# Performance work log

Hardware: AMD Instinct MI355X
Metric: run time of the kernel (lower is better)

The kernel has to match this reference:

```python
import jax, jax.numpy as jnp
import numpy as np

N_NODES = 100000
N_EDGES = 3200000
IN_CH = 128
HID_CH = 64
NEG_SLOPE = 0.2  # PyG GATConv default leaky_relu slope


def setup_inputs() -> dict:
    key = jax.random.key(0)
    k1, k2, k3, k4, k5, k6 = jax.random.split(key, 6)
    x = jax.random.normal(k1, (N_NODES, IN_CH), dtype=jnp.float32)
    edge_index = jax.random.randint(k2, (2, N_EDGES), 0, N_NODES, dtype=jnp.int64)
    # learned params of GATConv(in, hid, heads=1)
    W = jax.random.normal(k3, (IN_CH, HID_CH), dtype=jnp.float32) / np.sqrt(IN_CH)
    att_src = jax.random.normal(k4, (HID_CH,), dtype=jnp.float32) / np.sqrt(HID_CH)
    att_dst = jax.random.normal(k5, (HID_CH,), dtype=jnp.float32) / np.sqrt(HID_CH)
    bias = jax.random.normal(k6, (HID_CH,), dtype=jnp.float32) * 0.01
    return {"x": x, "edge_index": edge_index, "W": W, "att_src": att_src,
            "att_dst": att_dst, "bias": bias}


def reference(x, edge_index, W, att_src, att_dst, bias):
    N = x.shape[0]
    h = x @ W  # [N, H] linear transform
    # PyG GATConv default: add self loops
    loops = jnp.arange(N, dtype=edge_index.dtype)
    src = jnp.concatenate([edge_index[0], loops])  # [E+N]
    dst = jnp.concatenate([edge_index[1], loops])
    # per-node attention halves, then gather per-edge
    a_src = h @ att_src  # [N]
    a_dst = h @ att_dst  # [N]
    e = jax.nn.leaky_relu(a_src[src] + a_dst[dst], NEG_SLOPE)  # [E+N]
    # segment softmax over incoming edges of each destination node
    m = jax.ops.segment_max(e, dst, num_segments=N)
    e = jnp.exp(e - m[dst])
    s = jax.ops.segment_sum(e, dst, num_segments=N)
    alpha = e / s[dst]  # [E+N]
    # scatter-aggregate weighted source features
    out = jax.ops.segment_sum(h[src] * alpha[:, None], dst, num_segments=N) + bias
    return out, alpha[:, None]
```

## Files before the change

kernel.cpp:

```cpp
#include <hip/hip_runtime.h>
#include <hip/hip_bf16.h>

#define IN_CH 128
#define HID 64
#define NEG_SLOPE 0.2f
#define BSH 8
#define CAP 10240

typedef __attribute__((ext_vector_type(8))) short short8;
typedef __attribute__((ext_vector_type(4))) float floatx4;
typedef __attribute__((ext_vector_type(2))) float f32x2;

__device__ inline short bfr(float f) {
    unsigned u = __float_as_uint(f);
    u += 0x7fffu + ((u >> 16) & 1u);
    return (short)(u >> 16);
}

__global__ void k_prep(const float* __restrict__ W, short* __restrict__ wfrag,
                       int* __restrict__ g_cursor)
{
    if (blockIdx.x == 0) {
        g_cursor[threadIdx.x] = 0;
        g_cursor[threadIdx.x + 256] = 0;
    }
    int idx = blockIdx.x * 256 + threadIdx.x;
    if (idx >= 1024) return;
    int f = idx >> 6, l = idx & 63;
    int kt = f >> 2, nt = f & 3;
    int k0 = kt * 32 + (l >> 4) * 8;
    int n = nt * 16 + (l & 15);
#pragma unroll
    for (int j = 0; j < 8; ++j)
        wfrag[idx * 8 + j] = bfr(W[(k0 + j) * HID + n]);
}

__global__ __launch_bounds__(256) void k_gemm(
    const float* __restrict__ x, const short8* __restrict__ wfrag,
    const float* __restrict__ att_src, const float* __restrict__ att_dst,
    short* __restrict__ h, float* __restrict__ a_src,
    float* __restrict__ a_dst, int N)
{
    const int t = threadIdx.x;
    const int lane = t & 63;
    const int wv = t >> 6;
    const int l15 = lane & 15;
    const int quad = lane >> 4;

    short8 bf[16];
#pragma unroll
    for (int f = 0; f < 16; ++f) bf[f] = wfrag[f * 64 + lane];

    float as4[4], ad4[4];
#pragma unroll
    for (int nt = 0; nt < 4; ++nt) {
        as4[nt] = att_src[nt * 16 + l15];
        ad4[nt] = att_dst[nt * 16 + l15];
    }

    const int rowbase = blockIdx.x * 128 + wv * 32;

#pragma unroll
    for (int mt = 0; mt < 2; ++mt) {
        const int m0 = rowbase + mt * 16;
        const int rowa = m0 + l15;
        const int rowc = rowa < N ? rowa : N - 1;
        const float* xp = x + (size_t)rowc * IN_CH + quad * 8;

        short8 af[4];
#pragma unroll
        for (int kt = 0; kt < 4; ++kt) {
            float4 p0 = *(const float4*)(xp + kt * 32);
            float4 p1 = *(const float4*)(xp + kt * 32 + 4);
            short8 a;
            a[0] = bfr(p0.x); a[1] = bfr(p0.y); a[2] = bfr(p0.z); a[3] = bfr(p0.w);
            a[4] = bfr(p1.x); a[5] = bfr(p1.y); a[6] = bfr(p1.z); a[7] = bfr(p1.w);
            af[kt] = a;
        }

        floatx4 acc[4];
#pragma unroll
        for (int nt = 0; nt < 4; ++nt) acc[nt] = (floatx4){0.f, 0.f, 0.f, 0.f};
#pragma unroll
        for (int kt = 0; kt < 4; ++kt)
#pragma unroll
            for (int nt = 0; nt < 4; ++nt)
                acc[nt] = __builtin_amdgcn_mfma_f32_16x16x32_bf16(
                    af[kt], bf[kt * 4 + nt], acc[nt], 0, 0, 0);

#pragma unroll
        for (int r = 0; r < 4; ++r) {
            const int row = m0 + quad * 4 + r;
            const bool ok = row < N;
            if (ok) {
#pragma unroll
                for (int nt = 0; nt < 4; ++nt)
                    h[(size_t)row * HID + nt * 16 + l15] = bfr(acc[nt][r]);
            }
            float ps = acc[0][r] * as4[0] + acc[1][r] * as4[1] +
                       acc[2][r] * as4[2] + acc[3][r] * as4[3];
            float pd = acc[0][r] * ad4[0] + acc[1][r] * ad4[1] +
                       acc[2][r] * ad4[2] + acc[3][r] * ad4[3];
#pragma unroll
            for (int m2 = 1; m2 < 16; m2 <<= 1) {
                ps += __shfl_xor(ps, m2, 64);
                pd += __shfl_xor(pd, m2, 64);
            }
            if (ok && l15 == 0) { a_src[row] = ps; a_dst[row] = pd; }
        }
    }
}

__global__ __launch_bounds__(512) void k_binB(
    const int* __restrict__ ei, int* __restrict__ g_cursor,
    int* __restrict__ pairs, int E, int nb)
{
    __shared__ int hist[512];
    __shared__ int base[512];
    const int t = threadIdx.x;
    hist[t] = 0;
    __syncthreads();

    int s[8], d[8], l[8];
    const int4* s4 = (const int4*)ei;
    const int4* d4 = (const int4*)(ei + E);
    const int E4 = E >> 2;
    const int q0 = blockIdx.x * 1024;
#pragma unroll
    for (int i = 0; i < 2; ++i) {
        int q = q0 + i * 512 + t;
        int4 sv = make_int4(0, 0, 0, 0);
        int4 dv = make_int4(-1, -1, -1, -1);
        if (q < E4) { sv = s4[q]; dv = d4[q]; }
        s[4 * i + 0] = sv.x; s[4 * i + 1] = sv.y; s[4 * i + 2] = sv.z; s[4 * i + 3] = sv.w;
        d[4 * i + 0] = dv.x; d[4 * i + 1] = dv.y; d[4 * i + 2] = dv.z; d[4 * i + 3] = dv.w;
    }
#pragma unroll
    for (int i = 0; i < 8; ++i)
        if (d[i] >= 0) l[i] = atomicAdd(&hist[d[i] >> BSH], 1);
    __syncthreads();

    if (t < nb) base[t] = atomicAdd(&g_cursor[t], hist[t]);
    __syncthreads();

#pragma unroll
    for (int i = 0; i < 8; ++i) {
        if (d[i] < 0) continue;
        int b = d[i] >> BSH;
        int pos = base[b] + l[i];
        if (pos < CAP)
            pairs[b * CAP + pos] = s[i] | ((d[i] & 255) << 17);
    }
}

__global__ __launch_bounds__(512) void k_binC(
    const int* __restrict__ pairs, const int* __restrict__ g_cursor,
    int* __restrict__ row_start, int* __restrict__ cnt,
    int* __restrict__ csr_src, int N, int nb)
{
    __shared__ int h0[256];
    __shared__ int hs[512];
    __shared__ int cur[256];
    __shared__ int sbase;
    const int t = threadIdx.x;
    const int b = blockIdx.x;
    int m = g_cursor[b];
    if (m > CAP) m = CAP;
    const int4* pb4 = (const int4*)(pairs + b * CAP);
    const int m4 = (m + 3) >> 2;

    int bv = (t < nb) ? g_cursor[t] : 0;
    hs[t] = bv;
    __syncthreads();
    for (int off = 1; off < 512; off <<= 1) {
        int u = (t >= off) ? hs[t - off] : 0;
        __syncthreads();
        hs[t] += u;
        __syncthreads();
    }
    if (t == b) sbase = hs[t] - bv;
    if (t < 256) h0[t] = 0;
    __syncthreads();
    const int basec = sbase;

    for (int i4 = t; i4 < m4; i4 += 512) {
        const int4 p = pb4[i4];
        const int i = i4 << 2;
        if (i + 3 < m) {
            atomicAdd(&h0[p.x >> 17], 1);
            atomicAdd(&h0[p.y >> 17], 1);
            atomicAdd(&h0[p.z >> 17], 1);
            atomicAdd(&h0[p.w >> 17], 1);
        } else {
            if (i     < m) atomicAdd(&h0[p.x >> 17], 1);
            if (i + 1 < m) atomicAdd(&h0[p.y >> 17], 1);
            if (i + 2 < m) atomicAdd(&h0[p.z >> 17], 1);
        }
    }
    __syncthreads();

    if (t < 256) hs[t] = h0[t];
    __syncthreads();
    for (int off = 1; off < 256; off <<= 1) {
        int u = (t >= off && t < 256) ? hs[t - off] : 0;
        __syncthreads();
        if (t < 256) hs[t] += u;
        __syncthreads();
    }
    if (t < 256) {
        const int excl = hs[t] - h0[t];
        cur[t] = basec + excl;
        const int dd = (b << BSH) + t;
        if (dd < N) { row_start[dd] = basec + excl; cnt[dd] = h0[t]; }
    }
    __syncthreads();

    for (int i4 = t; i4 < m4; i4 += 512) {
        const int4 p = pb4[i4];
        const int i = i4 << 2;
        if (i < m) {
            int pos = atomicAdd(&cur[p.x >> 17], 1);
            csr_src[pos] = p.x & 0x1FFFF;
        }
        if (i + 1 < m) {
            int pos = atomicAdd(&cur[p.y >> 17], 1);
            csr_src[pos] = p.y & 0x1FFFF;
        }
        if (i + 2 < m) {
            int pos = atomicAdd(&cur[p.z >> 17], 1);
            csr_src[pos] = p.z & 0x1FFFF;
        }
        if (i + 3 < m) {
            int pos = atomicAdd(&cur[p.w >> 17], 1);
            csr_src[pos] = p.w & 0x1FFFF;
        }
    }
}

__global__ __launch_bounds__(256) void k_agg(
    const __hip_bfloat16* __restrict__ h, const float* __restrict__ a_src,
    const float* __restrict__ a_dst, const float* __restrict__ bias,
    const int* __restrict__ row_start, const int* __restrict__ cnt,
    const int* __restrict__ csr_src,
    float* __restrict__ out, float2* __restrict__ adi, int dbase, int N)
{
    __shared__ float red[4][2][576];

    const int wave = threadIdx.x >> 6;
    const int lane = threadIdx.x & 63;
    const int d0 = dbase + blockIdx.x * 8 + wave * 2;
    if (d0 >= N) return;
    const int d1 = d0 + 1;
    const bool has1 = d1 < N;

    const int q  = lane >> 3;
    const int i8 = lane & 7;

    const float2 ad2 = *(const float2*)(a_dst + d0);
    const float ad0 = ad2.x;
    const float ad1 = ad2.y;
    const int2 cn2 = *(const int2*)(cnt + d0);
    const int n0 = cn2.x;
    const int n1 = has1 ? cn2.y : 0;
    const int st0 = row_start[d0];
    const int en0 = st0 + n0;
    const int st1 = en0;
    const int en1 = st1 + n1;

    const uint4* h4 = (const uint4*)h;

    float ps0 = 0.f, ps1 = 0.f;
    f32x2 ac0[4], ac1[4];
#pragma unroll
    for (int c = 0; c < 4; ++c) {
        ac0[c] = (f32x2){0.f, 0.f};
        ac1[c] = (f32x2){0.f, 0.f};
    }

    const int nbt0 = (n0 + 63) >> 6;
    const int nbt1 = (n1 + 63) >> 6;
    const int nbm = nbt0 > nbt1 ? nbt0 : nbt1;

    int b0 = st0, b1 = st1;
    for (int it = 0; it < nbm; ++it, b0 += 64, b1 += 64) {
        int s0v = 0, s1v = 0;
        float e0 = 0.f, e1 = 0.f;
        const int idx0 = b0 + lane;
        if (it < nbt0 && idx0 < en0) {
            s0v = csr_src[idx0];
            float v = a_src[s0v] + ad0;
            v = v > 0.f ? v : NEG_SLOPE * v;
            e0 = __expf(v);
            ps0 += e0;
        }
        const int idx1 = b1 + lane;
        if (it < nbt1 && idx1 < en1) {
            s1v = csr_src[idx1];
            float v = a_src[s1v] + ad1;
            v = v > 0.f ? v : NEG_SLOPE * v;
            e1 = __expf(v);
            ps1 += e1;
        }
        const int m0 = (it < nbt0) ? min(64, en0 - b0) : 0;
        const int m1 = (it < nbt1) ? min(64, en1 - b1) : 0;
        const int mm = m0 > m1 ? m0 : m1;
#pragma unroll 4
        for (int j = 0; j < mm; j += 8) {
            const int jq = j + q;
            const int sj0 = __shfl(s0v, jq, 64);
            const float ej0 = __shfl(e0, jq, 64);
            const int sj1 = __shfl(s1v, jq, 64);
            const float ej1 = __shfl(e1, jq, 64);
            uint4 u0 = h4[(size_t)sj0 * 8 + i8];
            uint4 u1 = h4[(size_t)sj1 * 8 + i8];
            f32x2 ev0; ev0[0] = ej0; ev0[1] = ej0;
            f32x2 ev1; ev1[0] = ej1; ev1[1] = ej1;
            f32x2 c;
            c[0] = __uint_as_float(u0.x << 16);
            c[1] = __uint_as_float(u0.x & 0xffff0000u);
            ac0[0] = __builtin_elementwise_fma(ev0, c, ac0[0]);
            c[0] = __uint_as_float(u0.y << 16);
            c[1] = __uint_as_float(u0.y & 0xffff0000u);
            ac0[1] = __builtin_elementwise_fma(ev0, c, ac0[1]);
            c[0] = __uint_as_float(u0.z << 16);
            c[1] = __uint_as_float(u0.z & 0xffff0000u);
            ac0[2] = __builtin_elementwise_fma(ev0, c, ac0[2]);
            c[0] = __uint_as_float(u0.w << 16);
            c[1] = __uint_as_float(u0.w & 0xffff0000u);
            ac0[3] = __builtin_elementwise_fma(ev0, c, ac0[3]);
            c[0] = __uint_as_float(u1.x << 16);
            c[1] = __uint_as_float(u1.x & 0xffff0000u);
            ac1[0] = __builtin_elementwise_fma(ev1, c, ac1[0]);
            c[0] = __uint_as_float(u1.y << 16);
            c[1] = __uint_as_float(u1.y & 0xffff0000u);
            ac1[1] = __builtin_elementwise_fma(ev1, c, ac1[1]);
            c[0] = __uint_as_float(u1.z << 16);
            c[1] = __uint_as_float(u1.z & 0xffff0000u);
            ac1[2] = __builtin_elementwise_fma(ev1, c, ac1[2]);
            c[0] = __uint_as_float(u1.w << 16);
            c[1] = __uint_as_float(u1.w & 0xffff0000u);
            ac1[3] = __builtin_elementwise_fma(ev1, c, ac1[3]);
        }
    }

    float* r0 = &red[wave][0][0];
    float* r1 = &red[wave][1][0];
#pragma unroll
    for (int p = 0; p < 4; ++p) {
        r0[(i8 * 8 + 2 * p) * 9 + q]     = ac0[p][0];
        r0[(i8 * 8 + 2 * p + 1) * 9 + q] = ac0[p][1];
        r1[(i8 * 8 + 2 * p) * 9 + q]     = ac1[p][0];
        r1[(i8 * 8 + 2 * p + 1) * 9 + q] = ac1[p][1];
    }

#pragma unroll
    for (int m2 = 32; m2 > 0; m2 >>= 1) {
        ps0 += __shfl_xor(ps0, m2, 64);
        ps1 += __shfl_xor(ps1, m2, 64);
    }

    const float2 asd = *(const float2*)(a_src + d0);
    float vs0 = asd.x + ad0;
    vs0 = vs0 > 0.f ? vs0 : NEG_SLOPE * vs0;
    const float es0 = __expf(vs0);
    const float inv0 = 1.f / (ps0 + es0);
    float es1 = 0.f, inv1 = 0.f;
    if (has1) {
        float vs1 = asd.y + ad1;
        vs1 = vs1 > 0.f ? vs1 : NEG_SLOPE * vs1;
        es1 = __expf(vs1);
        inv1 = 1.f / (ps1 + es1);
    }
    if (lane == 0) {
        adi[d0] = make_float2(ad0, inv0);
        if (has1) adi[d1] = make_float2(ad1, inv1);
    }

    float s0 = 0.f, s1 = 0.f;
#pragma unroll
    for (int qq = 0; qq < 8; ++qq) {
        s0 += r0[lane * 9 + qq];
        s1 += r1[lane * 9 + qq];
    }

    const ushort* hu = (const ushort*)h;
    const float bi = bias[lane];
    float hs0 = __uint_as_float(((unsigned)hu[(size_t)d0 * HID + lane]) << 16);
    out[(size_t)d0 * HID + lane] = fmaf(es0, hs0, s0) * inv0 + bi;
    if (has1) {
        float hs1 = __uint_as_float(((unsigned)hu[(size_t)d1 * HID + lane]) << 16);
        out[(size_t)d1 * HID + lane] = fmaf(es1, hs1, s1) * inv1 + bi;
    }
}

__global__ void k_alpha(const int* __restrict__ ei,
                        const float* __restrict__ a_src,
                        const float2* __restrict__ adi,
                        float* __restrict__ out_alpha, int E, int N)
{
    const int E4 = E >> 2;
    const int i = blockIdx.x * 256 + threadIdx.x;
    if (i < E4) {
        const int4 sv = ((const int4*)ei)[i];
        const int4 dv = ((const int4*)(ei + E))[i];
        float4 o;
        {
            const float2 av = adi[dv.x];
            float v = a_src[sv.x] + av.x;
            v = v > 0.f ? v : NEG_SLOPE * v;
            o.x = __expf(v) * av.y;
        }
        {
            const float2 av = adi[dv.y];
            float v = a_src[sv.y] + av.x;
            v = v > 0.f ? v : NEG_SLOPE * v;
            o.y = __expf(v) * av.y;
        }
        {
            const float2 av = adi[dv.z];
            float v = a_src[sv.z] + av.x;
            v = v > 0.f ? v : NEG_SLOPE * v;
            o.z = __expf(v) * av.y;
        }
        {
            const float2 av = adi[dv.w];
            float v = a_src[sv.w] + av.x;
            v = v > 0.f ? v : NEG_SLOPE * v;
            o.w = __expf(v) * av.y;
        }
        ((float4*)out_alpha)[i] = o;
    } else {
        const int j = i - E4;
        if (j < N) {
            const float2 av = adi[j];
            float v = a_src[j] + av.x;
            v = v > 0.f ? v : NEG_SLOPE * v;
            out_alpha[E + j] = __expf(v) * av.y;
        }
    }
}

extern "C" void kernel_launch(void* const* d_in, const int* in_sizes, int n_in,
                              void* d_out, int out_size, void* d_ws, size_t ws_size,
                              hipStream_t stream)
{
    (void)n_in; (void)out_size; (void)ws_size;
    const float* x       = (const float*)d_in[0];
    const int*   ei      = (const int*)d_in[1];
    const float* W       = (const float*)d_in[2];
    const float* att_src = (const float*)d_in[3];
    const float* att_dst = (const float*)d_in[4];
    const float* bias    = (const float*)d_in[5];

    const int N = in_sizes[0] / IN_CH;
    const int E = in_sizes[1] / 2;
    const int nb = (N + 255) >> BSH;

    __hip_bfloat16* h = (__hip_bfloat16*)d_ws;
    float* a_src_d = (float*)(h + (size_t)N * HID);
    float* a_dst_d = a_src_d + N;
    float2* adi    = (float2*)(a_dst_d + N);
    int* row_start = (int*)(adi + N);
    int* cnt       = row_start + N;
    int* g_cursor  = cnt + N;
    short* wfrag   = (short*)(g_cursor + 512);
    int* pairs     = (int*)(wfrag + 8192);
    int* csr_src   = pairs + (size_t)nb * CAP;

    float* out       = (float*)d_out;
    float* out_alpha = out + (size_t)N * HID;

    k_prep<<<4, 256, 0, stream>>>(W, wfrag, g_cursor);
    k_gemm<<<(N + 127) / 128, 256, 0, stream>>>(x, (const short8*)wfrag,
                                                att_src, att_dst,
                                                (short*)h, a_src_d, a_dst_d, N);
    k_binB<<<(E / 4 + 1023) / 1024, 512, 0, stream>>>(ei, g_cursor, pairs, E, nb);
    k_binC<<<nb, 512, 0, stream>>>(pairs, g_cursor,
                                   row_start, cnt, csr_src, N, nb);

    const int H = 50000;
    k_agg<<<(H + 7) / 8, 256, 0, stream>>>(h, a_src_d, a_dst_d, bias,
                                           row_start, cnt, csr_src,
                                           out, adi, 0, H);
    k_agg<<<(N - H + 7) / 8, 256, 0, stream>>>(h, a_src_d, a_dst_d, bias,
                                               row_start, cnt, csr_src,
                                               out, adi, H, N);
    k_alpha<<<((E >> 2) + N + 255) / 256, 256, 0, stream>>>(ei, a_src_d, adi,
                                                            out_alpha, E, N);
}
```

Baseline: 275.9 us.

## Fuse GEMM and edge-binning kernels into one launch; merge split aggregation launches

The independent x@W GEMM and the edge-binning pass now run as two block ranges of a single 512-thread kernel, so they can execute concurrently and one launch is saved. The GEMM blocks now cover 256 rows each using 8 waves. The aggregation kernel, previously launched twice over node halves, is launched once over all nodes. This trades per-kernel specialization (launch bounds, register budget shared between two very different code paths) for fewer launches and overlap of compute-bound and atomic-bound work.

New measurement: 248.5 us. 9.9% less time.

```diff
diff --git a/kernel.cpp b/kernel.cpp
--- a/kernel.cpp
+++ b/kernel.cpp
@@ -35,121 +35,122 @@
         wfrag[idx * 8 + j] = bfr(W[(k0 + j) * HID + n]);
 }
 
-__global__ __launch_bounds__(256) void k_gemm(
+__global__ __launch_bounds__(512, 2) void k_gb(
     const float* __restrict__ x, const short8* __restrict__ wfrag,
     const float* __restrict__ att_src, const float* __restrict__ att_dst,
     short* __restrict__ h, float* __restrict__ a_src,
-    float* __restrict__ a_dst, int N)
-{
-    const int t = threadIdx.x;
-    const int lane = t & 63;
-    const int wv = t >> 6;
-    const int l15 = lane & 15;
-    const int quad = lane >> 4;
-
-    short8 bf[16];
-#pragma unroll
-    for (int f = 0; f < 16; ++f) bf[f] = wfrag[f * 64 + lane];
-
-    float as4[4], ad4[4];
-#pragma unroll
-    for (int nt = 0; nt < 4; ++nt) {
-        as4[nt] = att_src[nt * 16 + l15];
-        ad4[nt] = att_dst[nt * 16 + l15];
-    }
-
-    const int rowbase = blockIdx.x * 128 + wv * 32;
-
-#pragma unroll
-    for (int mt = 0; mt < 2; ++mt) {
-        const int m0 = rowbase + mt * 16;
-        const int rowa = m0 + l15;
-        const int rowc = rowa < N ? rowa : N - 1;
-        const float* xp = x + (size_t)rowc * IN_CH + quad * 8;
-
-        short8 af[4];
-#pragma unroll
-        for (int kt = 0; kt < 4; ++kt) {
-            float4 p0 = *(const float4*)(xp + kt * 32);
-            float4 p1 = *(const float4*)(xp + kt * 32 + 4);
-            short8 a;
-            a[0] = bfr(p0.x); a[1] = bfr(p0.y); a[2] = bfr(p0.z); a[3] = bfr(p0.w);
-            a[4] = bfr(p1.x); a[5] = bfr(p1.y); a[6] = bfr(p1.z); a[7] = bfr(p1.w);
-            af[kt] = a;
-        }
-
-        floatx4 acc[4];
-#pragma unroll
-        for (int nt = 0; nt < 4; ++nt) acc[nt] = (floatx4){0.f, 0.f, 0.f, 0.f};
-#pragma unroll
-        for (int kt = 0; kt < 4; ++kt)
-#pragma unroll
-            for (int nt = 0; nt < 4; ++nt)
-                acc[nt] = __builtin_amdgcn_mfma_f32_16x16x32_bf16(
-                    af[kt], bf[kt * 4 + nt], acc[nt], 0, 0, 0);
-
-#pragma unroll
-        for (int r = 0; r < 4; ++r) {
-            const int row = m0 + quad * 4 + r;
-            const bool ok = row < N;
-            if (ok) {
-#pragma unroll
-                for (int nt = 0; nt < 4; ++nt)
-                    h[(size_t)row * HID + nt * 16 + l15] = bfr(acc[nt][r]);
-            }
-            float ps = acc[0][r] * as4[0] + acc[1][r] * as4[1] +
-                       acc[2][r] * as4[2] + acc[3][r] * as4[3];
-            float pd = acc[0][r] * ad4[0] + acc[1][r] * ad4[1] +
-                       acc[2][r] * ad4[2] + acc[3][r] * ad4[3];
-#pragma unroll
-            for (int m2 = 1; m2 < 16; m2 <<= 1) {
-                ps += __shfl_xor(ps, m2, 64);
-                pd += __shfl_xor(pd, m2, 64);
-            }
-            if (ok && l15 == 0) { a_src[row] = ps; a_dst[row] = pd; }
-        }
-    }
-}
-
-__global__ __launch_bounds__(512) void k_binB(
+    float* __restrict__ a_dst,
     const int* __restrict__ ei, int* __restrict__ g_cursor,
-    int* __restrict__ pairs, int E, int nb)
+    int* __restrict__ pairs, int E, int N, int nb, int GB)
 {
     __shared__ int hist[512];
     __shared__ int base[512];
+
     const int t = threadIdx.x;
-    hist[t] = 0;
-    __syncthreads();
-
-    int s[8], d[8], l[8];
-    const int4* s4 = (const int4*)ei;
-    const int4* d4 = (const int4*)(ei + E);
-    const int E4 = E >> 2;
-    const int q0 = blockIdx.x * 1024;
-#pragma unroll
-    for (int i = 0; i < 2; ++i) {
-        int q = q0 + i * 512 + t;
-        int4 sv = make_int4(0, 0, 0, 0);
-        int4 dv = make_int4(-1, -1, -1, -1);
-        if (q < E4) { sv = s4[q]; dv = d4[q]; }
-        s[4 * i + 0] = sv.x; s[4 * i + 1] = sv.y; s[4 * i + 2] = sv.z; s[4 * i + 3] = sv.w;
-        d[4 * i + 0] = dv.x; d[4 * i + 1] = dv.y; d[4 * i + 2] = dv.z; d[4 * i + 3] = dv.w;
-    }
-#pragma unroll
-    for (int i = 0; i < 8; ++i)
-        if (d[i] >= 0) l[i] = atomicAdd(&hist[d[i] >> BSH], 1);
-    __syncthreads();
-
-    if (t < nb) base[t] = atomicAdd(&g_cursor[t], hist[t]);
-    __syncthreads();
-
-#pragma unroll
-    for (int i = 0; i < 8; ++i) {
-        if (d[i] < 0) continue;
-        int b = d[i] >> BSH;
-        int pos = base[b] + l[i];
-        if (pos < CAP)
-            pairs[b * CAP + pos] = s[i] | ((d[i] & 255) << 17);
+
+    if ((int)blockIdx.x < GB) {
+        const int lane = t & 63;
+        const int wv = t >> 6;
+        const int l15 = lane & 15;
+        const int quad = lane >> 4;
+
+        short8 bf[16];
+#pragma unroll
+        for (int f = 0; f < 16; ++f) bf[f] = wfrag[f * 64 + lane];
+
+        float as4[4], ad4[4];
+#pragma unroll
+        for (int nt = 0; nt < 4; ++nt) {
+            as4[nt] = att_src[nt * 16 + l15];
+            ad4[nt] = att_dst[nt * 16 + l15];
+        }
+
+        const int rowbase = blockIdx.x * 256 + wv * 32;
+
+#pragma unroll
+        for (int mt = 0; mt < 2; ++mt) {
+            const int m0 = rowbase + mt * 16;
+            const int rowa = m0 + l15;
+            const int rowc = rowa < N ? rowa : N - 1;
+            const float* xp = x + (size_t)rowc * IN_CH + quad * 8;
+
+            short8 af[4];
+#pragma unroll
+            for (int kt = 0; kt < 4; ++kt) {
+                float4 p0 = *(const float4*)(xp + kt * 32);
+                float4 p1 = *(const float4*)(xp + kt * 32 + 4);
+                short8 a;
+                a[0] = bfr(p0.x); a[1] = bfr(p0.y); a[2] = bfr(p0.z); a[3] = bfr(p0.w);
+                a[4] = bfr(p1.x); a[5] = bfr(p1.y); a[6] = bfr(p1.z); a[7] = bfr(p1.w);
+                af[kt] = a;
+            }
+
+            floatx4 acc[4];
+#pragma unroll
+            for (int nt = 0; nt < 4; ++nt) acc[nt] = (floatx4){0.f, 0.f, 0.f, 0.f};
+#pragma unroll
+            for (int kt = 0; kt < 4; ++kt)
+#pragma unroll
+                for (int nt = 0; nt < 4; ++nt)
+                    acc[nt] = __builtin_amdgcn_mfma_f32_16x16x32_bf16(
+                        af[kt], bf[kt * 4 + nt], acc[nt], 0, 0, 0);
+
+#pragma unroll
+            for (int r = 0; r < 4; ++r) {
+                const int row = m0 + quad * 4 + r;
+                const bool ok = row < N;
+                if (ok) {
+#pragma unroll
+                    for (int nt = 0; nt < 4; ++nt)
+                        h[(size_t)row * HID + nt * 16 + l15] = bfr(acc[nt][r]);
+                }
+                float ps = acc[0][r] * as4[0] + acc[1][r] * as4[1] +
+                           acc[2][r] * as4[2] + acc[3][r] * as4[3];
+                float pd = acc[0][r] * ad4[0] + acc[1][r] * ad4[1] +
+                           acc[2][r] * ad4[2] + acc[3][r] * ad4[3];
+#pragma unroll
+                for (int m2 = 1; m2 < 16; m2 <<= 1) {
+                    ps += __shfl_xor(ps, m2, 64);
+                    pd += __shfl_xor(pd, m2, 64);
+                }
+                if (ok && l15 == 0) { a_src[row] = ps; a_dst[row] = pd; }
+            }
+        }
+    } else {
+        const int bb = blockIdx.x - GB;
+        hist[t] = 0;
+        __syncthreads();
+
+        int s[8], d[8], l[8];
+        const int4* s4 = (const int4*)ei;
+        const int4* d4 = (const int4*)(ei + E);
+        const int E4 = E >> 2;
+        const int q0 = bb * 1024;
+#pragma unroll
+        for (int i = 0; i < 2; ++i) {
+            int q = q0 + i * 512 + t;
+            int4 sv = make_int4(0, 0, 0, 0);
+            int4 dv = make_int4(-1, -1, -1, -1);
+            if (q < E4) { sv = s4[q]; dv = d4[q]; }
+            s[4 * i + 0] = sv.x; s[4 * i + 1] = sv.y; s[4 * i + 2] = sv.z; s[4 * i + 3] = sv.w;
+            d[4 * i + 0] = dv.x; d[4 * i + 1] = dv.y; d[4 * i + 2] = dv.z; d[4 * i + 3] = dv.w;
+        }
+#pragma unroll
+        for (int i = 0; i < 8; ++i)
+            if (d[i] >= 0) l[i] = atomicAdd(&hist[d[i] >> BSH], 1);
+        __syncthreads();
+
+        if (t < nb) base[t] = atomicAdd(&g_cursor[t], hist[t]);
+        __syncthreads();
+
+#pragma unroll
+        for (int i = 0; i < 8; ++i) {
+            if (d[i] < 0) continue;
+            int b = d[i] >> BSH;
+            int pos = base[b] + l[i];
+            if (pos < CAP)
+                pairs[b * CAP + pos] = s[i] | ((d[i] & 255) << 17);
+        }
     }
 }
 
@@ -242,13 +243,13 @@
     const float* __restrict__ a_dst, const float* __restrict__ bias,
     const int* __restrict__ row_start, const int* __restrict__ cnt,
     const int* __restrict__ csr_src,
-    float* __restrict__ out, float2* __restrict__ adi, int dbase, int N)
+    float* __restrict__ out, float2* __restrict__ adi, int N)
 {
     __shared__ float red[4][2][576];
 
     const int wave = threadIdx.x >> 6;
     const int lane = threadIdx.x & 63;
-    const int d0 = dbase + blockIdx.x * 8 + wave * 2;
+    const int d0 = blockIdx.x * 8 + wave * 2;
     if (d0 >= N) return;
     const int d1 = d0 + 1;
     const bool has1 = d1 < N;
@@ -470,21 +471,19 @@
     float* out       = (float*)d_out;
     float* out_alpha = out + (size_t)N * HID;
 
+    const int GB = (N + 255) / 256;
+    const int BB = (E / 4 + 1023) / 1024;
+
     k_prep<<<4, 256, 0, stream>>>(W, wfrag, g_cursor);
-    k_gemm<<<(N + 127) / 128, 256, 0, stream>>>(x, (const short8*)wfrag,
-                                                att_src, att_dst,
-                                                (short*)h, a_src_d, a_dst_d, N);
-    k_binB<<<(E / 4 + 1023) / 1024, 512, 0, stream>>>(ei, g_cursor, pairs, E, nb);
+    k_gb<<<GB + BB, 512, 0, stream>>>(x, (const short8*)wfrag,
+                                      att_src, att_dst,
+                                      (short*)h, a_src_d, a_dst_d,
+                                      ei, g_cursor, pairs, E, N, nb, GB);
     k_binC<<<nb, 512, 0, stream>>>(pairs, g_cursor,
                                    row_start, cnt, csr_src, N, nb);
-
-    const int H = 50000;
-    k_agg<<<(H + 7) / 8, 256, 0, stream>>>(h, a_src_d, a_dst_d, bias,
+    k_agg<<<(N + 7) / 8, 256, 0, stream>>>(h, a_src_d, a_dst_d, bias,
                                            row_start, cnt, csr_src,
-                                           out, adi, 0, H);
-    k_agg<<<(N - H + 7) / 8, 256, 0, stream>>>(h, a_src_d, a_dst_d, bias,
-                                               row_start, cnt, csr_src,
-                                               out, adi, H, N);
+                                           out, adi, N);
     k_alpha<<<((E >> 2) + N + 255) / 256, 256, 0, stream>>>(ei, a_src_d, adi,
                                                             out_alpha, E, N);
 }
```
